# Optimization experiments

Hardware: AMD Instinct MI355X
Metric: run time of the kernel (lower is better)

Reference implementation:

```python
import jax, jax.numpy as jnp
import numpy as np

CIN, COUT, KH, KW = 128, 256, 3, 3

def setup_inputs() -> dict:
    key = jax.random.key(0)
    kx, kw = jax.random.split(key)
    x = jax.random.normal(kx, (32, CIN, 56, 56), dtype=jnp.float32)
    # kaiming normal, fan_in mode, relu gain: std = sqrt(2 / fan_in)
    fan_in = CIN * KH * KW
    weight = jax.random.normal(kw, (COUT, CIN, KH, KW), dtype=jnp.float32) * jnp.sqrt(2.0 / fan_in)
    bias = jnp.zeros((COUT,), dtype=jnp.float32)
    return {"x": x, "weight": weight, "bias": bias}

def reference(x, weight, bias):
    # VALID 2D cross-correlation (matches torch conv semantics of the manual loop)
    y = jax.lax.conv_general_dilated(
        x, weight,
        window_strides=(1, 1),
        padding="VALID",
        dimension_numbers=("NCHW", "OIHW", "NCHW"),
    )
    return y + bias[None, :, None, None]
```

## Files before the change

### kernel.cpp

```cpp
#include <hip/hip_runtime.h>
#include <hip/hip_bf16.h>

#define CIN 128
#define COUT 256
#define H 56
#define W 56
#define OH 54
#define OW 54

typedef __attribute__((ext_vector_type(8))) short short8;
typedef __attribute__((ext_vector_type(4))) float floatx4;

typedef __attribute__((address_space(3))) unsigned int  lds_u32;
typedef const __attribute__((address_space(1))) unsigned int glb_u32;

static __device__ __forceinline__ unsigned short f2bf(float f) {
  unsigned int u = __builtin_bit_cast(unsigned int, f);
  u += 0x7fffu + ((u >> 16) & 1u);
  return (unsigned short)(u >> 16);
}

__global__ void repack_w(const float* __restrict__ w, unsigned short* __restrict__ w2) {
  int idx = blockIdx.x * 256 + threadIdx.x;
  if (idx >= COUT * CIN * 9) return;
  int kw = idx % 3, t1 = idx / 3;
  int kh = t1 % 3, t2 = t1 / 3;
  int ci = t2 % CIN;
  int co = t2 / CIN;
  int c8 = ci >> 3, j = ci & 7;
  w2[((((kh * 3 + kw) * 16 + c8) * COUT + co) * 8) + j] = f2bf(w[idx]);
}

__global__ __launch_bounds__(256) void repack_x(const float* __restrict__ x,
                                                unsigned short* __restrict__ xb) {
  __shared__ float xt[56][129];
  const int h = blockIdx.x;
  const int n = blockIdx.y;
  const float* src = x + (size_t)n * CIN * (H * W) + h * W;
  #pragma unroll
  for (int r = 0; r < 28; ++r) {
    int idx = r * 256 + threadIdx.x;
    int ci = idx / 56, iw = idx % 56;
    xt[iw][ci] = src[ci * (H * W) + iw];
  }
  __syncthreads();
  unsigned short* dst = xb + ((size_t)n * H + h) * 896 * 8;
  #pragma unroll
  for (int r = 0; r < 4; ++r) {
    int g = r * 256 + threadIdx.x;
    if (g < 896) {
      int iw = g >> 4, c16 = g & 15;
      short8 v;
      #pragma unroll
      for (int j = 0; j < 8; ++j)
        v[j] = (short)f2bf(xt[iw][c16 * 8 + j]);
      int gp = iw * 16 + (c16 ^ (iw & 7));
      *reinterpret_cast<short8*>(&dst[gp * 8]) = v;
    }
  }
}

__global__ __launch_bounds__(256, 3) void conv6(
    const unsigned short* __restrict__ xb, const unsigned short* __restrict__ w2,
    const float* __restrict__ bias, float* __restrict__ out) {
  __shared__ alignas(16) unsigned short xs[2880 * 8];

  const int f = blockIdx.x;
  const int swz = (f & 7) * 216 + (f >> 3);
  const int oh = swz % 54;
  const int n  = swz / 54;
  const int tid  = threadIdx.x;
  const int wid  = tid >> 6;
  const int lane = tid & 63;
  const int l16  = lane & 15;
  const int cig  = lane >> 4;
  const int co_base = wid * 64;
  const int rowd = cig * 4;

  float bv[4][4];
  #pragma unroll
  for (int m = 0; m < 4; ++m)
    #pragma unroll
    for (int reg = 0; reg < 4; ++reg)
      bv[m][reg] = bias[co_base + m * 16 + rowd + reg];

  {
    const size_t gbase = ((size_t)n * H + oh) * 896;
    const size_t gmax  = (size_t)32 * H * 896 - 64;
    #pragma unroll
    for (int i = 0; i < 12; ++i) {
      int c = i * 4 + wid;
      if (c < 45) {
        size_t sg = gbase + (size_t)c * 64;
        if (sg > gmax) sg = gmax;
        __builtin_amdgcn_global_load_lds(
            (glb_u32*)(xb + (sg + lane) * 8),
            (lds_u32*)(&xs[(size_t)c * 64 * 8]), 16, 0, 0);
      }
    }
  }
  asm volatile("s_waitcnt vmcnt(0)" ::: "memory");
  __syncthreads();

  floatx4 acc[4][4];
  #pragma unroll
  for (int m = 0; m < 4; ++m)
    #pragma unroll
    for (int nr = 0; nr < 4; ++nr)
      acc[m][nr] = (floatx4){0.f, 0.f, 0.f, 0.f};

  #pragma unroll
  for (int s = 0; s < 36; ++s) {
    const int kh = s / 12, ch = (s / 3) & 3, kw = s % 3;
    const unsigned short* wp =
        w2 + ((size_t)(((kh * 3 + kw) * 16 + (ch * 4 + cig)) * COUT + co_base + l16)) * 8;
    short8 a[4];
    #pragma unroll
    for (int m = 0; m < 4; ++m)
      a[m] = *reinterpret_cast<const short8*>(wp + m * 128);
    const int iwl = l16 + kw;
    const int c16x = (ch * 4 + cig) ^ (iwl & 7);
    const int boff = (kh * 896 + iwl * 16 + c16x) * 8;
    short8 b[4];
    #pragma unroll
    for (int nr = 0; nr < 4; ++nr)
      b[nr] = *reinterpret_cast<const short8*>(&xs[boff + nr * 2048]);

    __builtin_amdgcn_s_setprio(1);
    #pragma unroll
    for (int m = 0; m < 4; ++m)
      #pragma unroll
      for (int nr = 0; nr < 4; ++nr)
        acc[m][nr] = __builtin_amdgcn_mfma_f32_16x16x32_bf16(a[m], b[nr], acc[m][nr], 0, 0, 0);
    __builtin_amdgcn_s_setprio(0);
  }

  #pragma unroll
  for (int m = 0; m < 4; ++m) {
    #pragma unroll
    for (int reg = 0; reg < 4; ++reg) {
      int co = co_base + m * 16 + rowd + reg;
      float* op = out + (((size_t)n * COUT + co) * OH + oh) * OW;
      #pragma unroll
      for (int nr = 0; nr < 4; ++nr) {
        int ow = nr * 16 + l16;
        if (ow < OW) op[ow] = acc[m][nr][reg] + bv[m][reg];
      }
    }
  }
}

#define CSTR 136
#define IWP 66

__global__ __launch_bounds__(512, 4) void conv_fb(
    const float* __restrict__ x, const unsigned short* __restrict__ w2,
    const float* __restrict__ bias, float* __restrict__ out) {
  __shared__ alignas(16) unsigned short xsf[4 * IWP * CSTR];

  const int ohp = blockIdx.x;
  const int n   = blockIdx.y;
  const int oh0 = ohp * 2;
  const int tid = threadIdx.x;

  {
    short8 zz = {0, 0, 0, 0, 0, 0, 0, 0};
    for (int i = tid; i < 4 * 10 * 17; i += 512) {
      int r = i / 170, rem = i % 170;
      int iw = 56 + rem / 17, g = rem % 17;
      *reinterpret_cast<short8*>(&xsf[(r * IWP + iw) * CSTR + g * 8]) = zz;
    }
  }
  for (int s = tid; s < 3584; s += 512) {
    int iw = s % 56;
    int t  = s / 56;
    int c8 = t & 15, r = t >> 4;
    const float* xp = x + (size_t)n * CIN * (H * W) + (oh0 + r) * W + iw;
    short8 v;
    #pragma unroll
    for (int j = 0; j < 8; ++j)
      v[j] = (short)f2bf(xp[(size_t)(c8 * 8 + j) * (H * W)]);
    *reinterpret_cast<short8*>(&xsf[(r * IWP + iw) * CSTR + c8 * 8]) = v;
  }
  __syncthreads();

  const int wid  = tid >> 6;
  const int lane = tid & 63;
  const int wm   = wid >> 1;
  const int wn   = wid & 1;
  const int l16  = lane & 15;
  const int cig  = lane >> 4;

  const int co_base = wm * 64;
  const int oh = oh0 + wn;

  floatx4 acc[4][4];
  #pragma unroll
  for (int m = 0; m < 4; ++m)
    #pragma unroll
    for (int nr = 0; nr < 4; ++nr)
      acc[m][nr] = (floatx4){0.f, 0.f, 0.f, 0.f};

  for (int kh = 0; kh < 3; ++kh) {
    const int row = wn + kh;
    #pragma unroll
    for (int ch = 0; ch < 4; ++ch) {
      const int bbase = (row * IWP + l16) * CSTR + ch * 32 + cig * 8;
      #pragma unroll
      for (int kw = 0; kw < 3; ++kw) {
        const unsigned short* wp =
            w2 + ((size_t)(((kh * 3 + kw) * 16 + (ch * 4 + cig)) * COUT + co_base + l16)) * 8;
        short8 a[4];
        #pragma unroll
        for (int m = 0; m < 4; ++m)
          a[m] = *reinterpret_cast<const short8*>(wp + m * 16 * 8);
        short8 b[4];
        #pragma unroll
        for (int nr = 0; nr < 4; ++nr)
          b[nr] = *reinterpret_cast<const short8*>(&xsf[bbase + (nr * 16 + kw) * CSTR]);
        #pragma unroll
        for (int m = 0; m < 4; ++m)
          #pragma unroll
          for (int nr = 0; nr < 4; ++nr)
            acc[m][nr] = __builtin_amdgcn_mfma_f32_16x16x32_bf16(a[m], b[nr], acc[m][nr], 0, 0, 0);
      }
    }
  }

  const int rowd = cig * 4;
  #pragma unroll
  for (int m = 0; m < 4; ++m) {
    #pragma unroll
    for (int reg = 0; reg < 4; ++reg) {
      int co = co_base + m * 16 + rowd + reg;
      float bvv = bias[co];
      float* op = out + (((size_t)n * COUT + co) * OH + oh) * OW;
      #pragma unroll
      for (int nr = 0; nr < 4; ++nr) {
        int ow = nr * 16 + l16;
        if (ow < OW) op[ow] = acc[m][nr][reg] + bvv;
      }
    }
  }
}

extern "C" void kernel_launch(void* const* d_in, const int* in_sizes, int n_in,
                              void* d_out, int out_size, void* d_ws, size_t ws_size,
                              hipStream_t stream) {
  (void)in_sizes; (void)n_in; (void)out_size;
  const float* x    = (const float*)d_in[0];
  const float* w    = (const float*)d_in[1];
  const float* bias = (const float*)d_in[2];
  float* out = (float*)d_out;

  const size_t W2_BYTES = (size_t)9 * 16 * COUT * 8 * 2;
  const size_t XB_BYTES = (size_t)32 * H * 896 * 8 * 2;
  unsigned short* w2 = (unsigned short*)d_ws;

  repack_w<<<dim3((COUT * CIN * 9 + 255) / 256), dim3(256), 0, stream>>>(w, w2);

  if (ws_size >= W2_BYTES + XB_BYTES) {
    unsigned short* xb = (unsigned short*)((char*)d_ws + W2_BYTES);
    repack_x<<<dim3(56, 32), dim3(256), 0, stream>>>(x, xb);
    conv6<<<dim3(1728), dim3(256), 0, stream>>>(xb, w2, bias, out);
  } else {
    conv_fb<<<dim3(27, 32), dim3(512), 0, stream>>>(x, w2, bias, out);
  }
}
```

Measured before the change: 93.04 us.

## Compute two output rows per block with 2x2 wave tiling of channels and rows

Each block now covers two output rows instead of one. It loads four input rows into LDS and arranges its four waves as 2 (output-channel halves of 128) x 2 (rows). Each wave holds 8x4 accumulators, so a weight fragment is reused across twice as many MFMAs and input rows shared by neighbouring outputs are loaded once. The cost is higher register pressure (occupancy hint lowered from 3 to 2 blocks per SM), more LDS per block, and half as many blocks (864).

```diff
diff --git a/kernel.cpp b/kernel.cpp
--- a/kernel.cpp
+++ b/kernel.cpp
@@ -60,51 +60,44 @@
   }
 }
 
-__global__ __launch_bounds__(256, 3) void conv6(
+__global__ __launch_bounds__(256, 2) void conv7(
     const unsigned short* __restrict__ xb, const unsigned short* __restrict__ w2,
     const float* __restrict__ bias, float* __restrict__ out) {
-  __shared__ alignas(16) unsigned short xs[2880 * 8];
+  __shared__ alignas(16) unsigned short xs[3744 * 8];
 
   const int f = blockIdx.x;
-  const int swz = (f & 7) * 216 + (f >> 3);
-  const int oh = swz % 54;
-  const int n  = swz / 54;
-  const int tid  = threadIdx.x;
+  const int swz = (f & 7) * 108 + (f >> 3);
+  const int ohp = swz % 27;
+  const int n   = swz / 27;
+  const int oh0 = ohp * 2;
+  const int tid = threadIdx.x;
   const int wid  = tid >> 6;
   const int lane = tid & 63;
+
+  {
+    const unsigned short* src = xb + ((size_t)n * H + oh0) * 896 * 8;
+    #pragma unroll
+    for (int i = 0; i < 14; ++i) {
+      int idx = (wid * 14 + i) * 64;
+      __builtin_amdgcn_global_load_lds(
+          (glb_u32*)(src + (size_t)(idx + lane) * 8),
+          (lds_u32*)(&xs[idx * 8]), 16, 0, 0);
+    }
+  }
+  asm volatile("s_waitcnt vmcnt(0)" ::: "memory");
+  __syncthreads();
+
+  const int wm   = wid >> 1;
+  const int wn   = wid & 1;
   const int l16  = lane & 15;
   const int cig  = lane >> 4;
-  const int co_base = wid * 64;
+  const int co_base = wm * 128;
+  const int oh = oh0 + wn;
   const int rowd = cig * 4;
 
-  float bv[4][4];
-  #pragma unroll
-  for (int m = 0; m < 4; ++m)
-    #pragma unroll
-    for (int reg = 0; reg < 4; ++reg)
-      bv[m][reg] = bias[co_base + m * 16 + rowd + reg];
-
-  {
-    const size_t gbase = ((size_t)n * H + oh) * 896;
-    const size_t gmax  = (size_t)32 * H * 896 - 64;
-    #pragma unroll
-    for (int i = 0; i < 12; ++i) {
-      int c = i * 4 + wid;
-      if (c < 45) {
-        size_t sg = gbase + (size_t)c * 64;
-        if (sg > gmax) sg = gmax;
-        __builtin_amdgcn_global_load_lds(
-            (glb_u32*)(xb + (sg + lane) * 8),
-            (lds_u32*)(&xs[(size_t)c * 64 * 8]), 16, 0, 0);
-      }
-    }
-  }
-  asm volatile("s_waitcnt vmcnt(0)" ::: "memory");
-  __syncthreads();
-
-  floatx4 acc[4][4];
-  #pragma unroll
-  for (int m = 0; m < 4; ++m)
+  floatx4 acc[8][4];
+  #pragma unroll
+  for (int m = 0; m < 8; ++m)
     #pragma unroll
     for (int nr = 0; nr < 4; ++nr)
       acc[m][nr] = (floatx4){0.f, 0.f, 0.f, 0.f};
@@ -112,15 +105,16 @@
   #pragma unroll
   for (int s = 0; s < 36; ++s) {
     const int kh = s / 12, ch = (s / 3) & 3, kw = s % 3;
+    const int row = wn + kh;
     const unsigned short* wp =
         w2 + ((size_t)(((kh * 3 + kw) * 16 + (ch * 4 + cig)) * COUT + co_base + l16)) * 8;
-    short8 a[4];
-    #pragma unroll
-    for (int m = 0; m < 4; ++m)
+    short8 a[8];
+    #pragma unroll
+    for (int m = 0; m < 8; ++m)
       a[m] = *reinterpret_cast<const short8*>(wp + m * 128);
     const int iwl = l16 + kw;
     const int c16x = (ch * 4 + cig) ^ (iwl & 7);
-    const int boff = (kh * 896 + iwl * 16 + c16x) * 8;
+    const int boff = (row * 896 + iwl * 16 + c16x) * 8;
     short8 b[4];
     #pragma unroll
     for (int nr = 0; nr < 4; ++nr)
@@ -128,7 +122,7 @@
 
     __builtin_amdgcn_s_setprio(1);
     #pragma unroll
-    for (int m = 0; m < 4; ++m)
+    for (int m = 0; m < 8; ++m)
       #pragma unroll
       for (int nr = 0; nr < 4; ++nr)
         acc[m][nr] = __builtin_amdgcn_mfma_f32_16x16x32_bf16(a[m], b[nr], acc[m][nr], 0, 0, 0);
@@ -136,15 +130,16 @@
   }
 
   #pragma unroll
-  for (int m = 0; m < 4; ++m) {
+  for (int m = 0; m < 8; ++m) {
     #pragma unroll
     for (int reg = 0; reg < 4; ++reg) {
       int co = co_base + m * 16 + rowd + reg;
+      float bvv = bias[co];
       float* op = out + (((size_t)n * COUT + co) * OH + oh) * OW;
       #pragma unroll
       for (int nr = 0; nr < 4; ++nr) {
         int ow = nr * 16 + l16;
-        if (ow < OW) op[ow] = acc[m][nr][reg] + bv[m][reg];
+        if (ow < OW) op[ow] = acc[m][nr][reg] + bvv;
       }
     }
   }
@@ -262,7 +257,7 @@
   if (ws_size >= W2_BYTES + XB_BYTES) {
     unsigned short* xb = (unsigned short*)((char*)d_ws + W2_BYTES);
     repack_x<<<dim3(56, 32), dim3(256), 0, stream>>>(x, xb);
-    conv6<<<dim3(1728), dim3(256), 0, stream>>>(xb, w2, bias, out);
+    conv7<<<dim3(864), dim3(256), 0, stream>>>(xb, w2, bias, out);
   } else {
     conv_fb<<<dim3(27, 32), dim3(512), 0, stream>>>(x, w2, bias, out);
   }
```

Measured after the change: 95.52 us. +2.7%, slower.
